# Performance work log

Hardware: AMD Instinct MI355X
Metric: run time of the kernel (lower is better)

## Reference

```python
import jax, jax.numpy as jnp
import numpy as np

SLIDING_WINDOW = 4
M = 450

def setup_inputs() -> dict:
    P, C, d = 256, 128, 128
    key = jax.random.key(0)
    ks = jax.random.split(key, 16)
    n = lambda k, shape: jax.random.normal(k, shape, dtype=jnp.float32)
    # Linear init scale ~ 1/sqrt(fan_in) to keep activations sane
    s_m = 1.0 / np.sqrt(M)
    return {
        "x": n(ks[0], (8, P, C)),
        "t": 8,
        "TwE": n(ks[1], (SLIDING_WINDOW, d)),
        "PE": n(ks[2], (P, d)),
        "CE": n(ks[3], (C, d)),
        "mE": n(ks[4], (M, d)),
        "ext_W1": n(ks[5], (M, M)) * s_m,
        "ext_b1": n(ks[6], (M,)) * s_m,
        "ext_W2": n(ks[7], (M, M)) * s_m,
        "ext_b2": n(ks[8], (M,)) * s_m,
        "dec_W1": n(ks[9], (M, M)) * s_m,
        "dec_b1": n(ks[10], (M,)) * s_m,
        "dec_W2": n(ks[11], (4 * P * C, M)) * s_m,
        "dec_b2": n(ks[12], (4 * P * C,)) * s_m,
    }

def reference(x, t, TwE, PE, CE, mE, ext_W1, ext_b1, ext_W2, ext_b2,
              dec_W1, dec_b1, dec_W2, dec_b2):
    P, C = PE.shape[0], CE.shape[0]
    xw = x[-SLIDING_WINDOW:]  # (4, P, C)
    # Factorized CP contraction: identical math to
    # einsum('ti,pi,ci,mi->tpcm') followed by einsum('tpcm,tpc->m'),
    # but reduces over t,p,c first without materializing the rank-4 tensor.
    f = jnp.einsum('tpc,ti,pi,ci->i', xw, TwE, PE, CE)  # (d,)
    feat = mE @ f  # (m,)
    # extractor_MLP: Linear(m,m) -> ReLU -> Linear(m,m)
    feat = ext_W2 @ jax.nn.relu(ext_W1 @ feat + ext_b1) + ext_b2
    # dec: Linear(m,m) -> ReLU -> Linear(m, 4*P*C)
    out = dec_W2 @ jax.nn.relu(dec_W1 @ feat + dec_b1) + dec_b2
    return out.reshape(4, P, C)
```

## Files before the change

### kernel.cpp

```cpp
#include <hip/hip_runtime.h>

#define WS_F     0
#define WS_FEAT0 128
#define WS_H1    640
#define WS_FEAT  1152
#define WS_H2    1664

__global__ __launch_bounds__(256) void k_f(
    const float* __restrict__ x, const float* __restrict__ TwE,
    const float* __restrict__ PE, const float* __restrict__ CE,
    float* __restrict__ f) {
  const int i = blockIdx.x;
  const int tid = threadIdx.x;
  __shared__ float sCE[128];
  __shared__ float sPE[256];
  __shared__ float sTw[4];
  __shared__ float coef[1024];
  __shared__ float red[4];
  if (tid < 128) sCE[tid] = CE[tid * 128 + i];
  sPE[tid] = PE[tid * 128 + i];
  if (tid < 4) sTw[tid] = TwE[tid * 128 + i];
  __syncthreads();
#pragma unroll
  for (int k = 0; k < 4; ++k) {
    int q = tid + (k << 8);
    coef[q] = sTw[q >> 8] * sPE[q & 255];
  }
  __syncthreads();
  const int lane = tid & 63;
  const int wv = tid >> 6;
  const float2 ce = ((const float2*)sCE)[lane];
  const float2* Xw = (const float2*)(x + 4 * 256 * 128);
  float acc = 0.f;
  const int q0 = wv * 256;
#pragma unroll 8
  for (int k = 0; k < 256; ++k) {
    int q = q0 + k;
    float2 v = Xw[q * 64 + lane];
    acc += coef[q] * (v.x * ce.x + v.y * ce.y);
  }
#pragma unroll
  for (int off = 32; off > 0; off >>= 1) acc += __shfl_down(acc, off);
  if (lane == 0) red[wv] = acc;
  __syncthreads();
  if (tid == 0) f[i] = red[0] + red[1] + red[2] + red[3];
}

__global__ __launch_bounds__(256) void k_mE(
    const float* __restrict__ mE, const float* __restrict__ f,
    float* __restrict__ feat0) {
  __shared__ float sf[128];
  const int tid = threadIdx.x;
  if (tid < 128) sf[tid] = f[tid];
  __syncthreads();
  const int lane = tid & 63;
  const int row = blockIdx.x * 4 + (tid >> 6);
  if (row >= 450) return;
  float2 v = ((const float2*)(mE + row * 128))[lane];
  float acc = v.x * sf[2 * lane] + v.y * sf[2 * lane + 1];
#pragma unroll
  for (int off = 32; off > 0; off >>= 1) acc += __shfl_down(acc, off);
  if (lane == 0) feat0[row] = acc;
}

__global__ __launch_bounds__(256) void k_mv450(
    const float* __restrict__ W, const float* __restrict__ b,
    const float* __restrict__ vin, float* __restrict__ vout, int relu) {
  __shared__ float sv[450];
  const int tid = threadIdx.x;
  if (tid < 450) sv[tid] = vin[tid];
  if (tid + 256 < 450) sv[tid + 256] = vin[tid + 256];
  __syncthreads();
  const int lane = tid & 63;
  const int row = blockIdx.x * 4 + (tid >> 6);
  if (row >= 450) return;
  const float2* Wr = (const float2*)(W + row * 450);
  float acc = 0.f;
#pragma unroll
  for (int k = 0; k < 4; ++k) {
    int idx = lane + k * 64;
    if (idx < 225) {
      float2 w = Wr[idx];
      acc += w.x * sv[2 * idx] + w.y * sv[2 * idx + 1];
    }
  }
#pragma unroll
  for (int off = 32; off > 0; off >>= 1) acc += __shfl_down(acc, off);
  if (lane == 0) {
    float r = acc + b[row];
    if (relu) r = fmaxf(r, 0.f);
    vout[row] = r;
  }
}

__global__ __launch_bounds__(256) void k_dec2(
    const float* __restrict__ W, const float* __restrict__ b,
    const float* __restrict__ h, float* __restrict__ out) {
  __shared__ float sv[450];
  const int tid = threadIdx.x;
  if (tid < 450) sv[tid] = h[tid];
  if (tid + 256 < 450) sv[tid + 256] = h[tid + 256];
  __syncthreads();
  const int lane = tid & 63;
  const int row = blockIdx.x * 4 + (tid >> 6);
  const float2* Wr = (const float2*)(W + (size_t)row * 450);
  float acc = 0.f;
#pragma unroll
  for (int k = 0; k < 4; ++k) {
    int idx = lane + k * 64;
    if (idx < 225) {
      float2 w = Wr[idx];
      acc += w.x * sv[2 * idx] + w.y * sv[2 * idx + 1];
    }
  }
#pragma unroll
  for (int off = 32; off > 0; off >>= 1) acc += __shfl_down(acc, off);
  if (lane == 0) out[row] = acc + b[row];
}

extern "C" void kernel_launch(void* const* d_in, const int* in_sizes, int n_in,
                              void* d_out, int out_size, void* d_ws, size_t ws_size,
                              hipStream_t stream) {
  const float* x   = (const float*)d_in[0];
  const float* TwE = (const float*)d_in[2];
  const float* PE  = (const float*)d_in[3];
  const float* CE  = (const float*)d_in[4];
  const float* mE  = (const float*)d_in[5];
  const float* eW1 = (const float*)d_in[6];
  const float* eb1 = (const float*)d_in[7];
  const float* eW2 = (const float*)d_in[8];
  const float* eb2 = (const float*)d_in[9];
  const float* dW1 = (const float*)d_in[10];
  const float* db1 = (const float*)d_in[11];
  const float* dW2 = (const float*)d_in[12];
  const float* db2 = (const float*)d_in[13];
  float* out = (float*)d_out;
  float* ws  = (float*)d_ws;

  k_f    <<<128,   256, 0, stream>>>(x, TwE, PE, CE, ws + WS_F);
  k_mE   <<<113,   256, 0, stream>>>(mE, ws + WS_F, ws + WS_FEAT0);
  k_mv450<<<113,   256, 0, stream>>>(eW1, eb1, ws + WS_FEAT0, ws + WS_H1, 1);
  k_mv450<<<113,   256, 0, stream>>>(eW2, eb2, ws + WS_H1, ws + WS_FEAT, 0);
  k_mv450<<<113,   256, 0, stream>>>(dW1, db1, ws + WS_FEAT, ws + WS_H2, 1);
  k_dec2 <<<32768, 256, 0, stream>>>(dW2, db2, ws + WS_H2, out);
}
```

Measured before the change: 377.2 us.

## Fuse front MLP stages into one persistent kernel and widen dec2 rows

Merges the five small front kernels (CP contraction, mE projection, three 450x450 matvecs) into one 128-block kernel that separates stages with an atomic-counter grid barrier, removing several launch gaps. The barrier counter is reset with a memset before each launch. The large decoder matvec now has each wavefront compute two adjacent output rows using float4 loads over a 900-float span, which halves the block count and widens memory accesses. The grid barrier depends on all 128 blocks being resident at the same time, which holds on this GPU but is not guaranteed in general.

```diff
diff --git a/kernel.cpp b/kernel.cpp
--- a/kernel.cpp
+++ b/kernel.cpp
@@ -5,117 +5,166 @@
 #define WS_H1    640
 #define WS_FEAT  1152
 #define WS_H2    1664
+#define WS_CNT   2176
 
-__global__ __launch_bounds__(256) void k_f(
-    const float* __restrict__ x, const float* __restrict__ TwE,
-    const float* __restrict__ PE, const float* __restrict__ CE,
-    float* __restrict__ f) {
-  const int i = blockIdx.x;
-  const int tid = threadIdx.x;
-  __shared__ float sCE[128];
-  __shared__ float sPE[256];
-  __shared__ float sTw[4];
-  __shared__ float coef[1024];
-  __shared__ float red[4];
-  if (tid < 128) sCE[tid] = CE[tid * 128 + i];
-  sPE[tid] = PE[tid * 128 + i];
-  if (tid < 4) sTw[tid] = TwE[tid * 128 + i];
+__device__ __forceinline__ void gbar(int* cnt, int target) {
   __syncthreads();
-#pragma unroll
-  for (int k = 0; k < 4; ++k) {
-    int q = tid + (k << 8);
-    coef[q] = sTw[q >> 8] * sPE[q & 255];
+  if (threadIdx.x == 0) {
+    __threadfence();
+    atomicAdd(cnt, 1);
+    while (__hip_atomic_load(cnt, __ATOMIC_RELAXED, __HIP_MEMORY_SCOPE_AGENT) < target) {
+      __builtin_amdgcn_s_sleep(8);
+    }
+    __threadfence();
   }
   __syncthreads();
-  const int lane = tid & 63;
-  const int wv = tid >> 6;
-  const float2 ce = ((const float2*)sCE)[lane];
-  const float2* Xw = (const float2*)(x + 4 * 256 * 128);
-  float acc = 0.f;
-  const int q0 = wv * 256;
-#pragma unroll 8
-  for (int k = 0; k < 256; ++k) {
-    int q = q0 + k;
-    float2 v = Xw[q * 64 + lane];
-    acc += coef[q] * (v.x * ce.x + v.y * ce.y);
-  }
-#pragma unroll
-  for (int off = 32; off > 0; off >>= 1) acc += __shfl_down(acc, off);
-  if (lane == 0) red[wv] = acc;
-  __syncthreads();
-  if (tid == 0) f[i] = red[0] + red[1] + red[2] + red[3];
 }
 
-__global__ __launch_bounds__(256) void k_mE(
-    const float* __restrict__ mE, const float* __restrict__ f,
-    float* __restrict__ feat0) {
-  __shared__ float sf[128];
-  const int tid = threadIdx.x;
-  if (tid < 128) sf[tid] = f[tid];
-  __syncthreads();
-  const int lane = tid & 63;
-  const int row = blockIdx.x * 4 + (tid >> 6);
-  if (row >= 450) return;
-  float2 v = ((const float2*)(mE + row * 128))[lane];
-  float acc = v.x * sf[2 * lane] + v.y * sf[2 * lane + 1];
-#pragma unroll
-  for (int off = 32; off > 0; off >>= 1) acc += __shfl_down(acc, off);
-  if (lane == 0) feat0[row] = acc;
-}
-
-__global__ __launch_bounds__(256) void k_mv450(
+__device__ __forceinline__ void phase_mv450(
     const float* __restrict__ W, const float* __restrict__ b,
-    const float* __restrict__ vin, float* __restrict__ vout, int relu) {
-  __shared__ float sv[450];
+    const float* __restrict__ vin, float* __restrict__ vout,
+    int relu, float* sv) {
   const int tid = threadIdx.x;
   if (tid < 450) sv[tid] = vin[tid];
   if (tid + 256 < 450) sv[tid + 256] = vin[tid + 256];
   __syncthreads();
   const int lane = tid & 63;
   const int row = blockIdx.x * 4 + (tid >> 6);
-  if (row >= 450) return;
-  const float2* Wr = (const float2*)(W + row * 450);
-  float acc = 0.f;
+  if (row < 450) {
+    const float2* Wr = (const float2*)(W + row * 450);
+    float acc = 0.f;
 #pragma unroll
-  for (int k = 0; k < 4; ++k) {
-    int idx = lane + k * 64;
-    if (idx < 225) {
-      float2 w = Wr[idx];
-      acc += w.x * sv[2 * idx] + w.y * sv[2 * idx + 1];
+    for (int k = 0; k < 4; ++k) {
+      int idx = lane + (k << 6);
+      if (idx < 225) {
+        float2 w = Wr[idx];
+        acc += w.x * sv[2 * idx] + w.y * sv[2 * idx + 1];
+      }
+    }
+#pragma unroll
+    for (int off = 32; off > 0; off >>= 1) acc += __shfl_down(acc, off);
+    if (lane == 0) {
+      float r = acc + b[row];
+      if (relu) r = fmaxf(r, 0.f);
+      vout[row] = r;
     }
   }
+}
+
+__global__ __launch_bounds__(256) void k_front(
+    const float* __restrict__ x, const float* __restrict__ TwE,
+    const float* __restrict__ PE, const float* __restrict__ CE,
+    const float* __restrict__ mE,
+    const float* __restrict__ eW1, const float* __restrict__ eb1,
+    const float* __restrict__ eW2, const float* __restrict__ eb2,
+    const float* __restrict__ dW1, const float* __restrict__ db1,
+    float* __restrict__ ws, int* __restrict__ cnt) {
+  __shared__ float smem[1416];
+  float* f     = ws + WS_F;
+  float* feat0 = ws + WS_FEAT0;
+  float* h1    = ws + WS_H1;
+  float* feat  = ws + WS_FEAT;
+  float* h2    = ws + WS_H2;
+  const int tid = threadIdx.x;
+  const int lane = tid & 63;
+
+  {
+    float* coef = smem;
+    float* sCE  = smem + 1024;
+    float* sPE  = smem + 1152;
+    float* sTw  = smem + 1408;
+    float* red  = smem + 1412;
+    const int i = blockIdx.x;
+    if (tid < 128) sCE[tid] = CE[tid * 128 + i];
+    sPE[tid] = PE[tid * 128 + i];
+    if (tid < 4) sTw[tid] = TwE[tid * 128 + i];
+    __syncthreads();
 #pragma unroll
-  for (int off = 32; off > 0; off >>= 1) acc += __shfl_down(acc, off);
-  if (lane == 0) {
-    float r = acc + b[row];
-    if (relu) r = fmaxf(r, 0.f);
-    vout[row] = r;
+    for (int k = 0; k < 4; ++k) {
+      int q = tid + (k << 8);
+      coef[q] = sTw[q >> 8] * sPE[q & 255];
+    }
+    __syncthreads();
+    const int wv = tid >> 6;
+    const float2 ce = ((const float2*)sCE)[lane];
+    const float2* Xw = (const float2*)(x + 4 * 256 * 128);
+    float acc = 0.f;
+    const int q0 = wv * 256;
+#pragma unroll 8
+    for (int k = 0; k < 256; ++k) {
+      int q = q0 + k;
+      float2 v = Xw[q * 64 + lane];
+      acc += coef[q] * (v.x * ce.x + v.y * ce.y);
+    }
+#pragma unroll
+    for (int off = 32; off > 0; off >>= 1) acc += __shfl_down(acc, off);
+    if (lane == 0) red[wv] = acc;
+    __syncthreads();
+    if (tid == 0) f[i] = red[0] + red[1] + red[2] + red[3];
   }
+  gbar(cnt, 128);
+
+  {
+    if (tid < 128) smem[tid] = f[tid];
+    __syncthreads();
+    const int row = blockIdx.x * 4 + (tid >> 6);
+    if (row < 450) {
+      float2 v = ((const float2*)(mE + row * 128))[lane];
+      float acc = v.x * smem[2 * lane] + v.y * smem[2 * lane + 1];
+#pragma unroll
+      for (int off = 32; off > 0; off >>= 1) acc += __shfl_down(acc, off);
+      if (lane == 0) feat0[row] = acc;
+    }
+  }
+  gbar(cnt, 256);
+
+  phase_mv450(eW1, eb1, feat0, h1, 1, smem);
+  gbar(cnt, 384);
+
+  phase_mv450(eW2, eb2, h1, feat, 0, smem);
+  gbar(cnt, 512);
+
+  phase_mv450(dW1, db1, feat, h2, 1, smem);
 }
 
 __global__ __launch_bounds__(256) void k_dec2(
     const float* __restrict__ W, const float* __restrict__ b,
     const float* __restrict__ h, float* __restrict__ out) {
-  __shared__ float sv[450];
+  __shared__ float sv2[900];
   const int tid = threadIdx.x;
-  if (tid < 450) sv[tid] = h[tid];
-  if (tid + 256 < 450) sv[tid + 256] = h[tid + 256];
+  for (int k = tid; k < 900; k += 256) sv2[k] = h[k < 450 ? k : k - 450];
   __syncthreads();
   const int lane = tid & 63;
-  const int row = blockIdx.x * 4 + (tid >> 6);
-  const float2* Wr = (const float2*)(W + (size_t)row * 450);
-  float acc = 0.f;
+  const int rp = blockIdx.x * 4 + (tid >> 6);
+  const float4* Wp = (const float4*)(W + (size_t)rp * 900);
+  float accA = 0.f, accB = 0.f;
 #pragma unroll
-  for (int k = 0; k < 4; ++k) {
-    int idx = lane + k * 64;
-    if (idx < 225) {
-      float2 w = Wr[idx];
-      acc += w.x * sv[2 * idx] + w.y * sv[2 * idx + 1];
-    }
+  for (int k = 0; k < 3; ++k) {
+    int j = lane + (k << 6);
+    float4 w = Wp[j];
+    const float* s = &sv2[4 * j];
+    float p01 = w.x * s[0] + w.y * s[1];
+    float p23 = w.z * s[2] + w.w * s[3];
+    if (4 * j + 3 < 450)      accA += p01 + p23;
+    else if (4 * j >= 450)    accB += p01 + p23;
+    else { accA += p01; accB += p23; }
+  }
+  if (lane < 33) {
+    int j = 192 + lane;
+    float4 w = Wp[j];
+    const float* s = &sv2[4 * j];
+    accB += w.x * s[0] + w.y * s[1] + w.z * s[2] + w.w * s[3];
   }
 #pragma unroll
-  for (int off = 32; off > 0; off >>= 1) acc += __shfl_down(acc, off);
-  if (lane == 0) out[row] = acc + b[row];
+  for (int off = 32; off > 0; off >>= 1) {
+    accA += __shfl_down(accA, off);
+    accB += __shfl_down(accB, off);
+  }
+  if (lane == 0) {
+    int r = rp * 2;
+    out[r]     = accA + b[r];
+    out[r + 1] = accB + b[r + 1];
+  }
 }
 
 extern "C" void kernel_launch(void* const* d_in, const int* in_sizes, int n_in,
@@ -136,11 +185,10 @@
   const float* db2 = (const float*)d_in[13];
   float* out = (float*)d_out;
   float* ws  = (float*)d_ws;
+  int* cnt   = (int*)(ws + WS_CNT);
 
-  k_f    <<<128,   256, 0, stream>>>(x, TwE, PE, CE, ws + WS_F);
-  k_mE   <<<113,   256, 0, stream>>>(mE, ws + WS_F, ws + WS_FEAT0);
-  k_mv450<<<113,   256, 0, stream>>>(eW1, eb1, ws + WS_FEAT0, ws + WS_H1, 1);
-  k_mv450<<<113,   256, 0, stream>>>(eW2, eb2, ws + WS_H1, ws + WS_FEAT, 0);
-  k_mv450<<<113,   256, 0, stream>>>(dW1, db1, ws + WS_FEAT, ws + WS_H2, 1);
-  k_dec2 <<<32768, 256, 0, stream>>>(dW2, db2, ws + WS_H2, out);
+  hipMemsetAsync((void*)cnt, 0, sizeof(int), stream);
+  k_front<<<128,   256, 0, stream>>>(x, TwE, PE, CE, mE, eW1, eb1, eW2, eb2,
+                                     dW1, db1, ws, cnt);
+  k_dec2 <<<16384, 256, 0, stream>>>(dW2, db2, ws + WS_H2, out);
 }
```

New measurement: 401.2 us. 6.4% more time.

## Process row pairs in decoder GEMV with 16-byte nontemporal weight loads

Applied to the files above, without the earlier changes.

The final decoder matrix-vector kernel now gives each wavefront two adjacent rows, treated as one contiguous 900-float span. This allows float4 loads instead of float2, and the shared vector is duplicated to match the span. Weight loads and output stores use nontemporal hints to avoid polluting cache with the 236MB streamed matrix. Splitting accumulators at the row boundary adds branchy per-lane logic, and half as many blocks are launched.

```diff
diff --git a/kernel.cpp b/kernel.cpp
--- a/kernel.cpp
+++ b/kernel.cpp
@@ -1,4 +1,6 @@
 #include <hip/hip_runtime.h>
+
+typedef float vf4 __attribute__((ext_vector_type(4)));
 
 #define WS_F     0
 #define WS_FEAT0 128
@@ -78,7 +80,7 @@
   float acc = 0.f;
 #pragma unroll
   for (int k = 0; k < 4; ++k) {
-    int idx = lane + k * 64;
+    int idx = lane + (k << 6);
     if (idx < 225) {
       float2 w = Wr[idx];
       acc += w.x * sv[2 * idx] + w.y * sv[2 * idx + 1];
@@ -96,26 +98,41 @@
 __global__ __launch_bounds__(256) void k_dec2(
     const float* __restrict__ W, const float* __restrict__ b,
     const float* __restrict__ h, float* __restrict__ out) {
-  __shared__ float sv[450];
+  __shared__ float sv2[900];
   const int tid = threadIdx.x;
-  if (tid < 450) sv[tid] = h[tid];
-  if (tid + 256 < 450) sv[tid + 256] = h[tid + 256];
+  for (int k = tid; k < 900; k += 256) sv2[k] = h[k < 450 ? k : k - 450];
   __syncthreads();
   const int lane = tid & 63;
-  const int row = blockIdx.x * 4 + (tid >> 6);
-  const float2* Wr = (const float2*)(W + (size_t)row * 450);
-  float acc = 0.f;
+  const int rp = blockIdx.x * 4 + (tid >> 6);
+  const vf4* Wp = (const vf4*)(W + (size_t)rp * 900);
+  float accA = 0.f, accB = 0.f;
 #pragma unroll
-  for (int k = 0; k < 4; ++k) {
-    int idx = lane + k * 64;
-    if (idx < 225) {
-      float2 w = Wr[idx];
-      acc += w.x * sv[2 * idx] + w.y * sv[2 * idx + 1];
-    }
+  for (int k = 0; k < 3; ++k) {
+    int j = lane + (k << 6);
+    vf4 w = __builtin_nontemporal_load(&Wp[j]);
+    const float* s = &sv2[4 * j];
+    float p01 = w.x * s[0] + w.y * s[1];
+    float p23 = w.z * s[2] + w.w * s[3];
+    if (4 * j + 3 < 450)      accA += p01 + p23;
+    else if (4 * j >= 450)    accB += p01 + p23;
+    else { accA += p01; accB += p23; }
+  }
+  if (lane < 33) {
+    int j = 192 + lane;
+    vf4 w = __builtin_nontemporal_load(&Wp[j]);
+    const float* s = &sv2[4 * j];
+    accB += w.x * s[0] + w.y * s[1] + w.z * s[2] + w.w * s[3];
   }
 #pragma unroll
-  for (int off = 32; off > 0; off >>= 1) acc += __shfl_down(acc, off);
-  if (lane == 0) out[row] = acc + b[row];
+  for (int off = 32; off > 0; off >>= 1) {
+    accA += __shfl_down(accA, off);
+    accB += __shfl_down(accB, off);
+  }
+  if (lane == 0) {
+    int r = rp * 2;
+    __builtin_nontemporal_store(accA + b[r],     &out[r]);
+    __builtin_nontemporal_store(accB + b[r + 1], &out[r + 1]);
+  }
 }
 
 extern "C" void kernel_launch(void* const* d_in, const int* in_sizes, int n_in,
@@ -142,5 +159,5 @@
   k_mv450<<<113,   256, 0, stream>>>(eW1, eb1, ws + WS_FEAT0, ws + WS_H1, 1);
   k_mv450<<<113,   256, 0, stream>>>(eW2, eb2, ws + WS_H1, ws + WS_FEAT, 0);
   k_mv450<<<113,   256, 0, stream>>>(dW1, db1, ws + WS_FEAT, ws + WS_H2, 1);
-  k_dec2 <<<32768, 256, 0, stream>>>(dW2, db2, ws + WS_H2, out);
+  k_dec2 <<<16384, 256, 0, stream>>>(dW2, db2, ws + WS_H2, out);
 }
```

New measurement: 374.7 us. Within noise of the previous version (-0.6%).
